# Performance work log

Hardware: AMD Instinct MI355X
Metric: run time of the kernel (lower is better)

## Reference

```python
import jax, jax.numpy as jnp
import numpy as np
from jax import lax

B, C_IN, C_OUT, RES, K = 2, 16, 32, 64, 3


def setup_inputs() -> dict:
    key = jax.random.key(0)
    kx, km, kw = jax.random.split(key, 3)
    x = jax.random.normal(kx, (B, C_IN, RES, RES, RES), dtype=jnp.float32)
    # the rest are exactly zero -> drives the nonzero-voxel masking path
    keep = jax.random.bernoulli(km, 0.3, (B, 1, RES, RES, RES))
    x = x * keep.astype(jnp.float32)
    # weight matches nn.Parameter(torch.randn(1, out_ch, in_ch, k, k, k))
    weight = jax.random.normal(kw, (1, C_OUT, C_IN, K, K, K), dtype=jnp.float32)
    return {"x": x, "weight": weight}


def reference(x, weight):
    # SparseConv3d: output at voxel v (for each out channel) is
    #   sum_{i, dx, dy, dz} padded_x[i, v+offset] * W[o, i, offset+pad]
    # evaluated ONLY where x has any nonzero channel; zero elsewhere.
    # This is a 'same'-padded cross-correlation masked by voxel occupancy.
    w = weight[0]  # [O, I, k, k, k]
    out = lax.conv_general_dilated(
        x, w,
        window_strides=(1, 1, 1),
        padding="SAME",
        dimension_numbers=("NCDHW", "OIDHW", "NCDHW"),
    )  # [B, O, D, H, W]
    occ = jnp.any(x != 0, axis=1, keepdims=True)  # [B,1,D,H,W] nonzero-voxel mask
    return out * occ.astype(out.dtype)
```

## Files before the change

### kernel.cpp

```cpp
#include <hip/hip_runtime.h>

#define RES   64
#define RES2  4096
#define RES3  262144
#define CIN   16
#define COUT  32

#define PZ 66
#define PY 66
#define ROWB  1088
#define XH16_BYTES (2*PZ*PY*2*ROWB)
#define NCHUNK (XH16_BYTES/16)
#define WTG_OFF ((XH16_BYTES + 255) & ~255)
#define NWH (27*CIN*COUT)

#define XT_BYTES (72*ROWB)
#define LDS_BYTES XT_BYTES

typedef _Float16 f16x8 __attribute__((ext_vector_type(8)));
typedef float   f32x16 __attribute__((ext_vector_type(16)));

static __device__ __forceinline__ unsigned int pack2(float v0, float v1) {
    _Float16 h0 = (_Float16)v0;
    _Float16 h1 = (_Float16)v1;
    unsigned short u0 = __builtin_bit_cast(unsigned short, h0);
    unsigned short u1 = __builtin_bit_cast(unsigned short, h1);
    return (unsigned int)u0 | ((unsigned int)u1 << 16);
}

typedef __attribute__((address_space(1))) const unsigned int gu32;
typedef __attribute__((address_space(3))) unsigned int lu32;
static __device__ __forceinline__ void glds16(const void* g, void* l) {
    __builtin_amdgcn_global_load_lds((gu32*)g, (lu32*)l, 16, 0, 0);
}

__global__ __launch_bounds__(256) void xcvt_kernel(
    const float* __restrict__ x, uint4* __restrict__ xh16,
    const float* __restrict__ w, _Float16* __restrict__ wtg) {

    if (blockIdx.x == 0) {
        for (int i = threadIdx.x; i < NWH; i += 256) {
            int tap = i >> 9;
            int hi  = (i >> 8) & 1;
            int o   = (i >> 3) & 31;
            int c   = i & 7;
            int ci  = hi * 8 + c;
            wtg[i] = (_Float16)w[(o * CIN + ci) * 27 + tap];
        }
    }

    for (int idx = blockIdx.x * 256 + threadIdx.x; idx < NCHUNK;
         idx += 2048 * 256) {
        int row = idx / 136;
        int rem = idx - row * 136;
        int hi  = rem / 68;
        int s   = rem - hi * 68;
        int y1  = row % 66;
        int t   = row / 66;
        int z1  = t % 66;
        int b   = t / 66;

        uint4 val = make_uint4(0u, 0u, 0u, 0u);
        if (z1 >= 1 && z1 <= 64 && y1 >= 1 && y1 <= 64 && s >= 1 && s <= 64) {
            const float* sp = x + ((size_t)(b * CIN + hi * 8)) * RES3
                                + (z1 - 1) * RES2 + (y1 - 1) * RES + (s - 1);
            val.x = pack2(sp[0 * RES3], sp[1 * RES3]);
            val.y = pack2(sp[2 * RES3], sp[3 * RES3]);
            val.z = pack2(sp[4 * RES3], sp[5 * RES3]);
            val.w = pack2(sp[6 * RES3], sp[7 * RES3]);
        }
        xh16[idx] = val;
    }
}

__global__ __launch_bounds__(512, 4) void conv_kernel(
    const char* __restrict__ xh16b, const char* __restrict__ wtgb,
    float* __restrict__ out) {

    extern __shared__ char smem[];
    char* xt = smem;

    int bid = blockIdx.x;
    int sb  = (bid & 7) * 64 + (bid >> 3);
    int b   = sb >> 8;
    int zt  = (sb >> 4) & 15;
    int yt  = sb & 15;
    int z0 = zt * 4, y0 = yt * 4;

    int tid  = threadIdx.x;
    int lane = tid & 63;
    int wv   = tid >> 6;
    int hi   = lane >> 5;
    int l31  = lane & 31;

    #pragma unroll
    for (int j = 0; j < 9; ++j) {
        int R   = wv * 9 + j;
        int iz  = R / 12;
        int rm  = R - iz * 12;
        int iy  = rm >> 1;
        int hh  = rm & 1;
        const char* srow = xh16b +
            ((((size_t)b * PZ + (z0 + iz)) * PY + (y0 + iy)) * 2 + hh) * (size_t)ROWB;
        char* drow = xt + R * ROWB;
        glds16(srow + lane * 16, drow);
        if (lane < 4) glds16(srow + 1024 + lane * 16, drow + 1024);
    }
    __syncthreads();

    int oy  = wv & 3;
    int oz0 = (wv >> 2) * 2;

    const int hb = hi * ROWB;
    const char* xbase = xt + hb + l31 * 16;
    const char* wtab  = wtgb + hi * 512 + l31 * 16;

    f32x16 acc00 = {};
    f32x16 acc01 = {};
    f32x16 acc10 = {};
    f32x16 acc11 = {};

    #pragma unroll
    for (int g = 0; g < 3; ++g) {
        #pragma unroll
        for (int dyp = 0; dyp < 3; ++dyp) {
            const char* wp = wtab + (size_t)(g * 9 + dyp * 3) * 1024;
            f16x8 wf0 = *(const f16x8*)(wp);
            f16x8 wf1 = *(const f16x8*)(wp + 1024);
            f16x8 wf2 = *(const f16x8*)(wp + 2048);
            const char* xrow = xbase + (((oz0 + g) * 6 + (oy + dyp)) * 2) * ROWB;
            #pragma unroll
            for (int dxp = 0; dxp < 3; ++dxp) {
                f16x8 wf = (dxp == 0) ? wf0 : ((dxp == 1) ? wf1 : wf2);
                f16x8 bA0 = *(const f16x8*)(xrow + dxp * 16);
                f16x8 bA1 = *(const f16x8*)(xrow + 512 + dxp * 16);
                f16x8 bB0 = *(const f16x8*)(xrow + 12 * ROWB + dxp * 16);
                f16x8 bB1 = *(const f16x8*)(xrow + 12 * ROWB + 512 + dxp * 16);
                acc00 = __builtin_amdgcn_mfma_f32_32x32x16_f16(wf, bA0, acc00, 0, 0, 0);
                acc01 = __builtin_amdgcn_mfma_f32_32x32x16_f16(wf, bA1, acc01, 0, 0, 0);
                acc10 = __builtin_amdgcn_mfma_f32_32x32x16_f16(wf, bB0, acc10, 0, 0, 0);
                acc11 = __builtin_amdgcn_mfma_f32_32x32x16_f16(wf, bB1, acc11, 0, 0, 0);
            }
        }
    }

    unsigned occm[2][2];
    #pragma unroll
    for (int ozo = 0; ozo < 2; ++ozo) {
        int R = (((oz0 + ozo + 1) * 6) + (oy + 1)) * 2;
        #pragma unroll
        for (int xh = 0; xh < 2; ++xh) {
            const char* mp = xt + R * ROWB + (xh * 32 + l31 + 1) * 16;
            uint4 a = *(const uint4*)(mp);
            uint4 c = *(const uint4*)(mp + ROWB);
            occm[ozo][xh] = (a.x | a.y | a.z | a.w | c.x | c.y | c.z | c.w) & 0x7FFF7FFFu;
        }
    }
    bool oA0 = occm[0][0] != 0u, oA1 = occm[0][1] != 0u;
    bool oB0 = occm[1][0] != 0u, oB1 = occm[1][1] != 0u;

    size_t vaddrA = (size_t)(z0 + oz0) * RES2 + (y0 + oy) * RES + l31;
    size_t vaddrB = vaddrA + RES2;

    #pragma unroll
    for (int r = 0; r < 16; ++r) {
        int o = (r & 3) + 8 * (r >> 2) + 4 * hi;
        float* pl = out + ((size_t)(b * COUT + o) << 18);
        pl[vaddrA]      = oA0 ? acc00[r] : 0.0f;
        pl[vaddrA + 32] = oA1 ? acc01[r] : 0.0f;
        pl[vaddrB]      = oB0 ? acc10[r] : 0.0f;
        pl[vaddrB + 32] = oB1 ? acc11[r] : 0.0f;
    }
}

extern "C" void kernel_launch(void* const* d_in, const int* in_sizes, int n_in,
                              void* d_out, int out_size, void* d_ws, size_t ws_size,
                              hipStream_t stream) {
    const float* x = (const float*)d_in[0];
    const float* w = (const float*)d_in[1];
    float* out = (float*)d_out;

    uint4*    xh16 = (uint4*)d_ws;
    _Float16* wtg  = (_Float16*)((char*)d_ws + WTG_OFF);

    (void)hipFuncSetAttribute(reinterpret_cast<const void*>(conv_kernel),
                              hipFuncAttributeMaxDynamicSharedMemorySize, LDS_BYTES);

    xcvt_kernel<<<2048, 256, 0, stream>>>(x, xh16, w, wtg);
    conv_kernel<<<512, 512, LDS_BYTES, stream>>>((const char*)xh16,
                                                 (const char*)wtg, out);
}
```

Measured before the change: 120.1 us.

## Fuse fp32-to-fp16 input conversion and padding into conv kernel halo load

Drops the separate pass that converted x into a padded, channel-interleaved fp16 buffer in workspace. The conv kernel now reads fp32 x directly from global memory, packs 16 channels to fp16, and writes them plus zero halo into LDS. A small kernel still transposes the weights. This removes a full write and re-read of the padded intermediate, at the cost of redundant halo loads across tiles and strided per-channel global reads inside the conv kernel.

```diff
diff --git a/kernel.cpp b/kernel.cpp
--- a/kernel.cpp
+++ b/kernel.cpp
@@ -5,15 +5,9 @@
 #define RES3  262144
 #define CIN   16
 #define COUT  32
-
-#define PZ 66
-#define PY 66
-#define ROWB  1088
-#define XH16_BYTES (2*PZ*PY*2*ROWB)
-#define NCHUNK (XH16_BYTES/16)
-#define WTG_OFF ((XH16_BYTES + 255) & ~255)
 #define NWH (27*CIN*COUT)
 
+#define ROWB  1088
 #define XT_BYTES (72*ROWB)
 #define LDS_BYTES XT_BYTES
 
@@ -28,53 +22,19 @@
     return (unsigned int)u0 | ((unsigned int)u1 << 16);
 }
 
-typedef __attribute__((address_space(1))) const unsigned int gu32;
-typedef __attribute__((address_space(3))) unsigned int lu32;
-static __device__ __forceinline__ void glds16(const void* g, void* l) {
-    __builtin_amdgcn_global_load_lds((gu32*)g, (lu32*)l, 16, 0, 0);
-}
-
-__global__ __launch_bounds__(256) void xcvt_kernel(
-    const float* __restrict__ x, uint4* __restrict__ xh16,
+__global__ __launch_bounds__(256) void wtrans_kernel(
     const float* __restrict__ w, _Float16* __restrict__ wtg) {
-
-    if (blockIdx.x == 0) {
-        for (int i = threadIdx.x; i < NWH; i += 256) {
-            int tap = i >> 9;
-            int hi  = (i >> 8) & 1;
-            int o   = (i >> 3) & 31;
-            int c   = i & 7;
-            int ci  = hi * 8 + c;
-            wtg[i] = (_Float16)w[(o * CIN + ci) * 27 + tap];
-        }
-    }
-
-    for (int idx = blockIdx.x * 256 + threadIdx.x; idx < NCHUNK;
-         idx += 2048 * 256) {
-        int row = idx / 136;
-        int rem = idx - row * 136;
-        int hi  = rem / 68;
-        int s   = rem - hi * 68;
-        int y1  = row % 66;
-        int t   = row / 66;
-        int z1  = t % 66;
-        int b   = t / 66;
-
-        uint4 val = make_uint4(0u, 0u, 0u, 0u);
-        if (z1 >= 1 && z1 <= 64 && y1 >= 1 && y1 <= 64 && s >= 1 && s <= 64) {
-            const float* sp = x + ((size_t)(b * CIN + hi * 8)) * RES3
-                                + (z1 - 1) * RES2 + (y1 - 1) * RES + (s - 1);
-            val.x = pack2(sp[0 * RES3], sp[1 * RES3]);
-            val.y = pack2(sp[2 * RES3], sp[3 * RES3]);
-            val.z = pack2(sp[4 * RES3], sp[5 * RES3]);
-            val.w = pack2(sp[6 * RES3], sp[7 * RES3]);
-        }
-        xh16[idx] = val;
-    }
+    int i = blockIdx.x * 256 + threadIdx.x;
+    if (i >= NWH) return;
+    int tap = i >> 9;
+    int hi  = (i >> 8) & 1;
+    int o   = (i >> 3) & 31;
+    int c   = i & 7;
+    wtg[i] = (_Float16)w[(o * CIN + hi * 8 + c) * 27 + tap];
 }
 
 __global__ __launch_bounds__(512, 4) void conv_kernel(
-    const char* __restrict__ xh16b, const char* __restrict__ wtgb,
+    const float* __restrict__ x, const char* __restrict__ wtgb,
     float* __restrict__ out) {
 
     extern __shared__ char smem[];
@@ -93,26 +53,45 @@
     int hi   = lane >> 5;
     int l31  = lane & 31;
 
+    const float* xb = x + (size_t)b * CIN * RES3;
+    const uint4 zz = make_uint4(0u, 0u, 0u, 0u);
     #pragma unroll
-    for (int j = 0; j < 9; ++j) {
-        int R   = wv * 9 + j;
-        int iz  = R / 12;
-        int rm  = R - iz * 12;
-        int iy  = rm >> 1;
-        int hh  = rm & 1;
-        const char* srow = xh16b +
-            ((((size_t)b * PZ + (z0 + iz)) * PY + (y0 + iy)) * 2 + hh) * (size_t)ROWB;
-        char* drow = xt + R * ROWB;
-        glds16(srow + lane * 16, drow);
-        if (lane < 4) glds16(srow + 1024 + lane * 16, drow + 1024);
+    for (int j = 0; j < 5; ++j) {
+        int p = wv + j * 8;
+        if (p >= 36) break;
+        int iz = p / 6, iy = p - iz * 6;
+        int gz = z0 + iz - 1, gy = y0 + iy - 1;
+        char* d0 = xt + (p * 2) * ROWB;
+        uint4 lo = zz, hh = zz;
+        if (((unsigned)gz < 64u) && ((unsigned)gy < 64u)) {
+            const float* sp = xb + gz * RES2 + gy * RES + lane;
+            float v0  = sp[0];          float v1  = sp[RES3];
+            float v2  = sp[2 * RES3];   float v3  = sp[3 * RES3];
+            float v4  = sp[4 * RES3];   float v5  = sp[5 * RES3];
+            float v6  = sp[6 * RES3];   float v7  = sp[7 * RES3];
+            float v8  = sp[8 * RES3];   float v9  = sp[9 * RES3];
+            float v10 = sp[10 * RES3];  float v11 = sp[11 * RES3];
+            float v12 = sp[12 * RES3];  float v13 = sp[13 * RES3];
+            float v14 = sp[14 * RES3];  float v15 = sp[15 * RES3];
+            lo = make_uint4(pack2(v0, v1),  pack2(v2, v3),
+                            pack2(v4, v5),  pack2(v6, v7));
+            hh = make_uint4(pack2(v8, v9),  pack2(v10, v11),
+                            pack2(v12, v13), pack2(v14, v15));
+        }
+        *(uint4*)(d0 + (lane + 1) * 16)        = lo;
+        *(uint4*)(d0 + ROWB + (lane + 1) * 16) = hh;
+        if (lane < 4) {
+            int cz = (lane == 0) ? 0 : (64 + lane);
+            *(uint4*)(d0 + cz * 16)        = zz;
+            *(uint4*)(d0 + ROWB + cz * 16) = zz;
+        }
     }
     __syncthreads();
 
     int oy  = wv & 3;
     int oz0 = (wv >> 2) * 2;
 
-    const int hb = hi * ROWB;
-    const char* xbase = xt + hb + l31 * 16;
+    const char* xbase = xt + hi * ROWB + l31 * 16;
     const char* wtab  = wtgb + hi * 512 + l31 * 16;
 
     f32x16 acc00 = {};
@@ -180,13 +159,11 @@
     const float* w = (const float*)d_in[1];
     float* out = (float*)d_out;
 
-    uint4*    xh16 = (uint4*)d_ws;
-    _Float16* wtg  = (_Float16*)((char*)d_ws + WTG_OFF);
+    _Float16* wtg = (_Float16*)d_ws;
 
     (void)hipFuncSetAttribute(reinterpret_cast<const void*>(conv_kernel),
                               hipFuncAttributeMaxDynamicSharedMemorySize, LDS_BYTES);
 
-    xcvt_kernel<<<2048, 256, 0, stream>>>(x, xh16, w, wtg);
-    conv_kernel<<<512, 512, LDS_BYTES, stream>>>((const char*)xh16,
-                                                 (const char*)wtg, out);
+    wtrans_kernel<<<(NWH + 255) / 256, 256, 0, stream>>>(w, wtg);
+    conv_kernel<<<512, 512, LDS_BYTES, stream>>>(x, (const char*)wtg, out);
 }
```

Result: faster. 101.9 us (-15.1%).
